# Kernel tuning notes

Measured on AMD Instinct MI355X. Metric: run time of the kernel, lower is better.

The kernel has to match this reference:

```python
import jax, jax.numpy as jnp
import numpy as np

C = 512
NUM_HEADS = 8
NUM_GROUPS = 32
EPS = 1e-6


def group_norm(x, gamma, beta):
    # x: [B, C, N]
    b, c, n = x.shape
    xg = x.reshape(b, NUM_GROUPS, (c // NUM_GROUPS) * n)
    mean = xg.mean(axis=-1, keepdims=True)
    var = xg.var(axis=-1, keepdims=True)
    xg = (xg - mean) * jax.lax.rsqrt(var + EPS)
    x = xg.reshape(b, c, n)
    return x * gamma[None, :, None] + beta[None, :, None]


def conv1x1(x, w, bias):
    # pointwise conv: w [out_c, in_c], x [B, C, N]
    return jnp.einsum('oc,bcn->bon', w, x) + bias[None, :, None]


def setup_inputs() -> dict:
    key = jax.random.key(0)
    ks = jax.random.split(key, 11)
    s = 1.0 / np.sqrt(C)
    inp = {
        'x': jax.random.normal(ks[0], (4, C, 2048), dtype=jnp.float32),
        'gn_gamma': jnp.ones((C,), jnp.float32),
        'gn_beta': jnp.zeros((C,), jnp.float32),
        'q_w': jax.random.uniform(ks[1], (C, C), jnp.float32, -s, s),
        'q_b': jax.random.uniform(ks[2], (C,), jnp.float32, -s, s),
        'k_w': jax.random.uniform(ks[3], (C, C), jnp.float32, -s, s),
        'k_b': jax.random.uniform(ks[4], (C,), jnp.float32, -s, s),
        'v_w': jax.random.uniform(ks[5], (C, C), jnp.float32, -s, s),
        'v_b': jax.random.uniform(ks[6], (C,), jnp.float32, -s, s),
        'proj_w': jax.random.uniform(ks[7], (C, C), jnp.float32, -s, s),
        'proj_b': jax.random.uniform(ks[8], (C,), jnp.float32, -s, s),
    }
    return inp


def reference(x, gn_gamma, gn_beta, q_w, q_b, k_w, k_b, v_w, v_b, proj_w, proj_b):
    b, c, n = x.shape
    hc = c // NUM_HEADS
    h_ = group_norm(x, gn_gamma, gn_beta)
    q = conv1x1(h_, q_w, q_b)
    k = conv1x1(h_, k_w, k_b)
    v = conv1x1(h_, v_w, v_b)
    # split heads: [B, H, hc, N]
    q = q.reshape(b, NUM_HEADS, hc, n)
    k = k.reshape(b, NUM_HEADS, hc, n)
    v = v.reshape(b, NUM_HEADS, hc, n)
    # NOTE: scale uses full channel count c, matching the original code
    scale = jnp.asarray(c, x.dtype) ** -0.5
    # scores: [B, H, Nq, Nk]
    w = jnp.einsum('bhcn,bhcm->bhnm', q, k) * scale
    w = jax.nn.softmax(w, axis=-1)
    # out[b,h,c,q] = sum_m v[b,h,c,m] * w[b,h,q,m]
    out = jnp.einsum('bhcm,bhqm->bhcq', v, w)
    out = out.reshape(b, c, n)
    out = conv1x1(out, proj_w, proj_b)
    return x + out
```

## Files before the change

### kernel.cpp

```cpp
#include <hip/hip_runtime.h>
#include <hip/hip_bf16.h>
#include <math.h>

#define C_DIM 512
#define N_DIM 2048
#define B_DIM 4
#define NGRP 32
#define GCH 16
#define NHEAD 8
#define HDIM 64
#define EPSV 1e-6f

using f32x4  = __attribute__((ext_vector_type(4))) float;
using bf16x8 = __attribute__((ext_vector_type(8))) short;

#define GLL16(gp, lp) __builtin_amdgcn_global_load_lds( \
    (const __attribute__((address_space(1))) unsigned int*)(gp), \
    (__attribute__((address_space(3))) unsigned int*)(lp), 16, 0, 0)

#define BFPACK(a, b) __builtin_amdgcn_perm(__float_as_uint(b), __float_as_uint(a), 0x07060302u)

static __device__ __forceinline__ unsigned short f2bf(float f) {
    union { __hip_bfloat16 h; unsigned short u; } cv;
    cv.h = __float2bfloat16(f);
    return cv.u;
}

__global__ __launch_bounds__(256) void gn_stats(const float* __restrict__ x,
                                                float* __restrict__ partial) {
    const int HSZ = GCH * N_DIM / 2;
    int blk = blockIdx.x;
    const float4* x4 = (const float4*)(x + (size_t)blk * HSZ);
    int tid = threadIdx.x;

    float s = 0.f, ss = 0.f;
    #pragma unroll
    for (int it = 0; it < HSZ / 4 / 256; ++it) {
        float4 v = x4[tid + it * 256];
        s  += v.x + v.y + v.z + v.w;
        ss += v.x * v.x + v.y * v.y + v.z * v.z + v.w * v.w;
    }
    __shared__ float rs[256], rss[256];
    rs[tid] = s; rss[tid] = ss;
    __syncthreads();
    for (int off = 128; off > 0; off >>= 1) {
        if (tid < off) { rs[tid] += rs[tid + off]; rss[tid] += rss[tid + off]; }
        __syncthreads();
    }
    if (tid == 0) {
        partial[blk * 2]     = rs[0];
        partial[blk * 2 + 1] = rss[0];
    }
}

__global__ __launch_bounds__(256) void gn_apply_t(const float* __restrict__ x,
                                                  const float* __restrict__ partial,
                                                  const float* __restrict__ gamma,
                                                  const float* __restrict__ beta,
                                                  unsigned short* __restrict__ ht) {
    __shared__ char smem[8192];
    const float GSZI = 1.f / (GCH * N_DIM);
    int n0 = blockIdx.x * 64, c0 = blockIdx.y * 64, b = blockIdx.z;
    int tid = threadIdx.x;
    #pragma unroll
    for (int it = 0; it < 4; ++it) {
        int idx = tid + it * 256;
        int ci = idx >> 4, n4 = (idx & 15) << 2;
        int cg = c0 + ci, grp = cg >> 4;
        int bg = b * NGRP + grp;
        float s  = partial[bg * 4]     + partial[bg * 4 + 2];
        float ss = partial[bg * 4 + 1] + partial[bg * 4 + 3];
        float mean = s * GSZI;
        float var  = ss * GSZI - mean * mean;
        float rstd = rsqrtf(var + EPSV);
        float ga = gamma[cg] * rstd, be = beta[cg] - mean * ga;
        float4 v = *(const float4*)&x[((size_t)b * C_DIM + cg) * N_DIM + n0 + n4];
        float vals[4] = {v.x, v.y, v.z, v.w};
        #pragma unroll
        for (int j = 0; j < 4; ++j) {
            int nl = n4 + j;
            *(unsigned short*)(smem + nl * 128 + ((ci * 2) ^ ((nl & 7) << 4))) =
                f2bf(vals[j] * ga + be);
        }
    }
    __syncthreads();
    #pragma unroll
    for (int i = 0; i < 2; ++i) {
        int idx = tid + i * 256;
        int row = idx >> 3, ch = idx & 7;
        bf16x8 v = *(const bf16x8*)(smem + row * 128 + ((ch * 16) ^ ((row & 7) << 4)));
        *(bf16x8*)&ht[((size_t)(b * N_DIM + n0 + row)) * C_DIM + c0 + ch * 8] = v;
    }
}

__global__ __launch_bounds__(256) void cast4_bf16(const float* __restrict__ s0,
                                                  const float* __restrict__ s1,
                                                  const float* __restrict__ s2,
                                                  const float* __restrict__ s3,
                                                  unsigned short* __restrict__ dst) {
    int which = blockIdx.y;
    const float* src = (which == 0) ? s0 : (which == 1) ? s1 : (which == 2) ? s2 : s3;
    size_t idx = (size_t)blockIdx.x * 256 + threadIdx.x;
    const float4* s4 = (const float4*)src;
    float4 a = s4[idx * 2], b = s4[idx * 2 + 1];
    bf16x8 o;
    o[0] = (short)f2bf(a.x); o[1] = (short)f2bf(a.y);
    o[2] = (short)f2bf(a.z); o[3] = (short)f2bf(a.w);
    o[4] = (short)f2bf(b.x); o[5] = (short)f2bf(b.y);
    o[6] = (short)f2bf(b.z); o[7] = (short)f2bf(b.w);
    *(bf16x8*)&dst[(size_t)which * 262144 + idx * 8] = o;
}

__global__ __launch_bounds__(512) void conv_qkv(const unsigned short* __restrict__ Wall,
                                                const float* __restrict__ q_b,
                                                const float* __restrict__ k_b,
                                                const float* __restrict__ v_b,
                                                const unsigned short* __restrict__ ht,
                                                unsigned short* __restrict__ qt,
                                                unsigned short* __restrict__ kt,
                                                unsigned short* __restrict__ vt,
                                                float escale) {
    __shared__ char smem[40960];

    int bn0 = blockIdx.x * 128;
    int bo  = blockIdx.y * 64;
    int tid = threadIdx.x;
    int L = tid & 63, w = tid >> 6;
    int g = L >> 4, c = L & 15;
    int wr = w >> 2, wc = w & 3;

    f32x4 acc[3][2][2];
    #pragma unroll
    for (int w3 = 0; w3 < 3; ++w3)
        #pragma unroll
        for (int t = 0; t < 2; ++t)
            #pragma unroll
            for (int u = 0; u < 2; ++u) acc[w3][t][u] = f32x4{0.f, 0.f, 0.f, 0.f};

    for (int k0 = 0; k0 < C_DIM; k0 += 64) {
        if (w < 4) {
            #pragma unroll
            for (int i = 0; i < 4; ++i) {
                int j = w * 4 + i;
                int row = j * 8 + (L >> 3);
                int sl = (L & 7) ^ (row & 7);
                GLL16(ht + (size_t)(bn0 + row) * C_DIM + k0 + sl * 8, smem + j * 1024);
            }
        } else {
            #pragma unroll
            for (int i = 0; i < 6; ++i) {
                int j = (w - 4) * 6 + i;
                int w3 = j >> 3, jj = j & 7;
                int row = jj * 8 + (L >> 3);
                int sl = (L & 7) ^ (row & 7);
                GLL16(Wall + (size_t)w3 * 262144 + (size_t)(bo + row) * C_DIM + k0 + sl * 8,
                      smem + 16384 + j * 1024);
            }
        }
        __syncthreads();

        bf16x8 bfr[2][2];
        #pragma unroll
        for (int u = 0; u < 2; ++u) {
            int row = wc * 32 + u * 16 + c;
            #pragma unroll
            for (int ks = 0; ks < 2; ++ks)
                bfr[u][ks] = *(const bf16x8*)(smem + row * 128 +
                                              ((g * 16 + ks * 64) ^ ((row & 7) << 4)));
        }
        #pragma unroll
        for (int w3 = 0; w3 < 3; ++w3) {
            char* As = smem + 16384 + w3 * 8192;
            bf16x8 af[2][2];
            #pragma unroll
            for (int t = 0; t < 2; ++t) {
                int row = wr * 32 + t * 16 + c;
                #pragma unroll
                for (int ks = 0; ks < 2; ++ks)
                    af[t][ks] = *(const bf16x8*)(As + row * 128 +
                                                 ((g * 16 + ks * 64) ^ ((row & 7) << 4)));
            }
            #pragma unroll
            for (int ks = 0; ks < 2; ++ks)
                #pragma unroll
                for (int t = 0; t < 2; ++t)
                    #pragma unroll
                    for (int u = 0; u < 2; ++u)
                        acc[w3][t][u] = __builtin_amdgcn_mfma_f32_16x16x32_bf16(
                            af[t][ks], bfr[u][ks], acc[w3][t][u], 0, 0, 0);
        }
        __syncthreads();
    }

    int b  = bn0 >> 11;
    int nb = bn0 & (N_DIM - 1);
    int hh = bo >> 6;
    int bh = b * NHEAD + hh;

    #pragma unroll
    for (int t = 0; t < 2; ++t)
        #pragma unroll
        for (int r = 0; r < 4; ++r) {
            int m = bo + wr * 32 + t * 16 + g * 4 + r;
            float bi = v_b[m];
            #pragma unroll
            for (int u = 0; u < 2; ++u) {
                int n = nb + wc * 32 + u * 16 + c;
                vt[((size_t)b * C_DIM + m) * N_DIM + n] = f2bf(acc[2][t][u][r] + bi);
            }
        }

    char* Ts = smem;
    #pragma unroll
    for (int pass = 0; pass < 2; ++pass) {
        const float* bias = pass ? k_b : q_b;
        float esc = pass ? 1.0f : escale;
        unsigned short* dst = pass ? kt : qt;
        __syncthreads();
        #pragma unroll
        for (int t = 0; t < 2; ++t)
            #pragma unroll
            for (int r = 0; r < 4; ++r) {
                int ml = wr * 32 + t * 16 + g * 4 + r;
                float bi = bias[bo + ml];
                #pragma unroll
                for (int u = 0; u < 2; ++u) {
                    int nl = wc * 32 + u * 16 + c;
                    *(unsigned short*)(Ts + nl * 128 + ((ml * 2) ^ ((nl & 7) << 4))) =
                        f2bf((acc[pass][t][u][r] + bi) * esc);
                }
            }
        __syncthreads();
        #pragma unroll
        for (int i = 0; i < 2; ++i) {
            int idx = tid + i * 512;
            int row = idx >> 3, ch = idx & 7;
            bf16x8 v = *(const bf16x8*)(Ts + row * 128 + ((ch * 16) ^ ((row & 7) << 4)));
            *(bf16x8*)&dst[((size_t)bh * N_DIM + nb + row) * HDIM + ch * 8] = v;
        }
    }
}

__global__ __launch_bounds__(256) void conv_proj(const unsigned short* __restrict__ Wb,
                                                 const float* __restrict__ bias,
                                                 const unsigned short* __restrict__ Bsrc,
                                                 const float* __restrict__ res,
                                                 float* __restrict__ outf) {
    __shared__ char smem[24576];
    int bn0 = blockIdx.x * 128;
    int bo  = blockIdx.y * 64;
    int tid = threadIdx.x;
    int L = tid & 63, w = tid >> 6;
    int g = L >> 4, c = L & 15;
    int wr = w >> 1, wc = w & 1;

    f32x4 acc[2][4];
    #pragma unroll
    for (int t = 0; t < 2; ++t)
        #pragma unroll
        for (int u = 0; u < 4; ++u) acc[t][u] = f32x4{0.f, 0.f, 0.f, 0.f};

    for (int k0 = 0; k0 < C_DIM; k0 += 64) {
        #pragma unroll
        for (int i = 0; i < 2; ++i) {
            int j = w * 2 + i;
            int ra = j * 8 + (L >> 3);
            int sl = (L & 7) ^ (ra & 7);
            GLL16(Wb + (size_t)(bo + ra) * C_DIM + k0 + sl * 8, smem + j * 1024);
        }
        #pragma unroll
        for (int i = 0; i < 4; ++i) {
            int j = w * 4 + i;
            int rb = j * 8 + (L >> 3);
            int sl = (L & 7) ^ (rb & 7);
            GLL16(Bsrc + (size_t)(bn0 + rb) * C_DIM + k0 + sl * 8, smem + 8192 + j * 1024);
        }
        __syncthreads();

        bf16x8 af[2][2], bfr[4][2];
        #pragma unroll
        for (int t = 0; t < 2; ++t) {
            int row = wr * 32 + t * 16 + c;
            #pragma unroll
            for (int ks = 0; ks < 2; ++ks)
                af[t][ks] = *(const bf16x8*)(smem + row * 128 +
                                             ((g * 16 + ks * 64) ^ ((row & 7) << 4)));
        }
        #pragma unroll
        for (int u = 0; u < 4; ++u) {
            int row = wc * 64 + u * 16 + c;
            #pragma unroll
            for (int ks = 0; ks < 2; ++ks)
                bfr[u][ks] = *(const bf16x8*)(smem + 8192 + row * 128 +
                                              ((g * 16 + ks * 64) ^ ((row & 7) << 4)));
        }
        #pragma unroll
        for (int ks = 0; ks < 2; ++ks)
            #pragma unroll
            for (int t = 0; t < 2; ++t)
                #pragma unroll
                for (int u = 0; u < 4; ++u)
                    acc[t][u] = __builtin_amdgcn_mfma_f32_16x16x32_bf16(
                        af[t][ks], bfr[u][ks], acc[t][u], 0, 0, 0);
        __syncthreads();
    }

    int b  = bn0 >> 11;
    int nb = bn0 & (N_DIM - 1);
    #pragma unroll
    for (int t = 0; t < 2; ++t)
        #pragma unroll
        for (int r = 0; r < 4; ++r) {
            int m = bo + wr * 32 + t * 16 + g * 4 + r;
            float bi = bias[m];
            #pragma unroll
            for (int u = 0; u < 4; ++u) {
                int n = nb + wc * 64 + u * 16 + c;
                size_t off = ((size_t)b * C_DIM + m) * N_DIM + n;
                outf[off] = acc[t][u][r] + bi + res[off];
            }
        }
}

__global__ __launch_bounds__(512, 4) void attn_kernel(const unsigned short* __restrict__ Qt,
                                                      const unsigned short* __restrict__ Kt,
                                                      const unsigned short* __restrict__ Vt,
                                                      unsigned short* __restrict__ at) {
    __shared__ char smem[49152];

    int d = blockIdx.x;
    int xcd = d & 7;
    int slot = d >> 3;
    int bh = xcd + 8 * (slot >> 4);
    int q0 = (slot & 15) * 128;

    int b = bh >> 3, hh = bh & 7;
    int tid = threadIdx.x;
    int L = tid & 63, w = tid >> 6;
    int g = L >> 4, c = L & 15;

    const unsigned short* Qh = Qt + (size_t)bh * N_DIM * HDIM;
    const unsigned short* Kh = Kt + (size_t)bh * N_DIM * HDIM;
    const unsigned short* Vh = Vt + (size_t)bh * HDIM * N_DIM;

    #pragma unroll
    for (int i = 0; i < 2; ++i) {
        int j = w * 2 + i;
        int row = j * 8 + (L >> 3);
        int sl = (L & 7) ^ (row & 7);
        GLL16(Qh + (size_t)(q0 + row) * HDIM + sl * 8, smem + j * 1024);
    }
    int srow = w * 8 + (L >> 3);
    int ssl  = (L & 7) ^ (srow & 7);
    GLL16(Kh + (size_t)srow * HDIM + ssl * 8, smem + 16384 + w * 1024);
    GLL16(Vh + (size_t)srow * N_DIM + ssl * 8, smem + 24576 + w * 1024);
    __syncthreads();

    int csw = (c & 7) << 4;
    char* kb0 = smem + 16384 + c * 128 + ((g * 16) ^ csw);
    char* kb1 = smem + 16384 + c * 128 + ((g * 16 + 64) ^ csw);
    char* pb  = smem + (w * 16 + c) * 128;
    char* pw0 = pb + ((g * 8) ^ csw);
    char* pw1 = pb + ((32 + g * 8) ^ csw);
    char* pw2 = pb + ((64 + g * 8) ^ csw);
    char* pw3 = pb + ((96 + g * 8) ^ csw);
    char* pr0 = pb + ((g * 16) ^ csw);
    char* pr1 = pb + ((64 + g * 16) ^ csw);

    bf16x8 qf[2];
    qf[0] = *(const bf16x8*)pr0;
    qf[1] = *(const bf16x8*)pr1;

    const unsigned short* kgp = Kh + (size_t)(64 + srow) * HDIM + ssl * 8;
    const unsigned short* vgp = Vh + (size_t)srow * N_DIM + 64 + ssl * 8;

    f32x4 oacc[4];
    #pragma unroll
    for (int t = 0; t < 4; ++t) oacc[t] = f32x4{0.f, 0.f, 0.f, 0.f};
    float m_r = -INFINITY, l_part = 0.f;

    auto tile = [&](int BOFF) {
        f32x4 sacc[4];
        #pragma unroll
        for (int t = 0; t < 4; ++t) sacc[t] = f32x4{0.f, 0.f, 0.f, 0.f};
        __builtin_amdgcn_s_setprio(1);
        #pragma unroll
        for (int t = 0; t < 4; ++t) {
            bf16x8 kf0 = *(const bf16x8*)(kb0 + BOFF + t * 2048);
            bf16x8 kf1 = *(const bf16x8*)(kb1 + BOFF + t * 2048);
            sacc[t] = __builtin_amdgcn_mfma_f32_16x16x32_bf16(kf0, qf[0], sacc[t], 0, 0, 0);
            sacc[t] = __builtin_amdgcn_mfma_f32_16x16x32_bf16(kf1, qf[1], sacc[t], 0, 0, 0);
        }
        __builtin_amdgcn_s_setprio(0);

        float t0 = fmaxf(fmaxf(sacc[0][0], sacc[0][1]), sacc[0][2]);
        float t1 = fmaxf(fmaxf(sacc[0][3], sacc[1][0]), sacc[1][1]);
        float t2 = fmaxf(fmaxf(sacc[1][2], sacc[1][3]), sacc[2][0]);
        float t3 = fmaxf(fmaxf(sacc[2][1], sacc[2][2]), sacc[2][3]);
        float t4 = fmaxf(fmaxf(sacc[3][0], sacc[3][1]), sacc[3][2]);
        float mloc = fmaxf(fmaxf(fmaxf(t0, t1), fmaxf(t2, t3)), fmaxf(t4, sacc[3][3]));
        if (!__all(mloc - m_r <= 6.0f)) {
            mloc = fmaxf(mloc, __shfl_xor(mloc, 16));
            mloc = fmaxf(mloc, __shfl_xor(mloc, 32));
            float mn = fmaxf(m_r, mloc);
            float fac = exp2f(m_r - mn);
            m_r = mn;
            l_part *= fac;
            #pragma unroll
            for (int t = 0; t < 4; ++t) oacc[t] = oacc[t] * fac;
        }
        f32x4 m4 = {m_r, m_r, m_r, m_r};
        f32x4 p[4];
        #pragma unroll
        for (int t = 0; t < 4; ++t) {
            f32x4 dd = sacc[t] - m4;
            p[t][0] = exp2f(dd[0]);
            p[t][1] = exp2f(dd[1]);
            p[t][2] = exp2f(dd[2]);
            p[t][3] = exp2f(dd[3]);
        }
        f32x4 racc = (p[0] + p[1]) + (p[2] + p[3]);
        l_part += (racc[0] + racc[1]) + (racc[2] + racc[3]);

        unsigned pk[4][2];
        #pragma unroll
        for (int t = 0; t < 4; ++t) {
            pk[t][0] = BFPACK(p[t][0], p[t][1]);
            pk[t][1] = BFPACK(p[t][2], p[t][3]);
        }

        *(unsigned long long*)pw0 = (unsigned long long)pk[0][0] | ((unsigned long long)pk[0][1] << 32);
        *(unsigned long long*)pw1 = (unsigned long long)pk[1][0] | ((unsigned long long)pk[1][1] << 32);
        *(unsigned long long*)pw2 = (unsigned long long)pk[2][0] | ((unsigned long long)pk[2][1] << 32);
        *(unsigned long long*)pw3 = (unsigned long long)pk[3][0] | ((unsigned long long)pk[3][1] << 32);

        __builtin_amdgcn_s_setprio(1);
        {
            bf16x8 pf0 = *(const bf16x8*)pr0;
            #pragma unroll
            for (int t = 0; t < 4; ++t) {
                bf16x8 vf = *(const bf16x8*)(kb0 + BOFF + 8192 + t * 2048);
                oacc[t] = __builtin_amdgcn_mfma_f32_16x16x32_bf16(vf, pf0, oacc[t], 0, 0, 0);
            }
            bf16x8 pf1 = *(const bf16x8*)pr1;
            #pragma unroll
            for (int t = 0; t < 4; ++t) {
                bf16x8 vf = *(const bf16x8*)(kb1 + BOFF + 8192 + t * 2048);
                oacc[t] = __builtin_amdgcn_mfma_f32_16x16x32_bf16(vf, pf1, oacc[t], 0, 0, 0);
            }
        }
        __builtin_amdgcn_s_setprio(0);
    };

    for (int i = 0; i < 16; ++i) {
        GLL16(kgp, smem + 32768 + w * 1024);
        GLL16(vgp, smem + 40960 + w * 1024);
        kgp += 64 * HDIM;
        vgp += 64;
        tile(0);
        __syncthreads();
        if (i < 15) {
            GLL16(kgp, smem + 16384 + w * 1024);
            GLL16(vgp, smem + 24576 + w * 1024);
            kgp += 64 * HDIM;
            vgp += 64;
        }
        tile(16384);
        __syncthreads();
    }

    float l_r = l_part;
    l_r += __shfl_xor(l_r, 16);
    l_r += __shfl_xor(l_r, 32);
    float oinv = 1.f / l_r;
    {
        unsigned lo, hi;
        lo = BFPACK(oacc[0][0] * oinv, oacc[0][1] * oinv);
        hi = BFPACK(oacc[0][2] * oinv, oacc[0][3] * oinv);
        *(unsigned long long*)pw0 = (unsigned long long)lo | ((unsigned long long)hi << 32);
        lo = BFPACK(oacc[1][0] * oinv, oacc[1][1] * oinv);
        hi = BFPACK(oacc[1][2] * oinv, oacc[1][3] * oinv);
        *(unsigned long long*)pw1 = (unsigned long long)lo | ((unsigned long long)hi << 32);
        lo = BFPACK(oacc[2][0] * oinv, oacc[2][1] * oinv);
        hi = BFPACK(oacc[2][2] * oinv, oacc[2][3] * oinv);
        *(unsigned long long*)pw2 = (unsigned long long)lo | ((unsigned long long)hi << 32);
        lo = BFPACK(oacc[3][0] * oinv, oacc[3][1] * oinv);
        hi = BFPACK(oacc[3][2] * oinv, oacc[3][3] * oinv);
        *(unsigned long long*)pw3 = (unsigned long long)lo | ((unsigned long long)hi << 32);
    }
    char* wbase = smem + w * 2048;
    #pragma unroll
    for (int i = 0; i < 2; ++i) {
        int idx = L + i * 64;
        int row = idx >> 3, ch = idx & 7;
        bf16x8 v = *(const bf16x8*)(wbase + row * 128 + ((ch * 16) ^ ((row & 7) << 4)));
        *(bf16x8*)&at[((size_t)(b * N_DIM + q0 + w * 16 + row)) * C_DIM + hh * HDIM + ch * 8] = v;
    }
}

extern "C" void kernel_launch(void* const* d_in, const int* in_sizes, int n_in,
                              void* d_out, int out_size, void* d_ws, size_t ws_size,
                              hipStream_t stream) {
    (void)in_sizes; (void)n_in; (void)out_size; (void)ws_size;
    const float* x     = (const float*)d_in[0];
    const float* gam   = (const float*)d_in[1];
    const float* bet   = (const float*)d_in[2];
    const float* q_w   = (const float*)d_in[3];
    const float* q_b   = (const float*)d_in[4];
    const float* k_w   = (const float*)d_in[5];
    const float* k_b   = (const float*)d_in[6];
    const float* v_w   = (const float*)d_in[7];
    const float* v_b   = (const float*)d_in[8];
    const float* p_w   = (const float*)d_in[9];
    const float* p_b   = (const float*)d_in[10];
    float* out = (float*)d_out;

    const size_t MB = 1 << 20;
    char* wsb = (char*)d_ws;
    unsigned short* ht  = (unsigned short*)(wsb);
    unsigned short* wqb = (unsigned short*)(wsb + 8 * MB);
    unsigned short* wpb = (unsigned short*)(wsb + 9 * MB + 512 * 1024);
    float*          partial = (float*)(wsb + 10 * MB);
    unsigned short* qt  = (unsigned short*)(wsb + 11 * MB);
    unsigned short* kt  = (unsigned short*)(wsb + 19 * MB);
    unsigned short* vt  = (unsigned short*)(wsb + 27 * MB);
    unsigned short* at  = (unsigned short*)(wsb + 35 * MB);

    gn_stats<<<B_DIM * NGRP * 2, 256, 0, stream>>>(x, partial);
    gn_apply_t<<<dim3(N_DIM / 64, C_DIM / 64, B_DIM), 256, 0, stream>>>(x, partial, gam, bet, ht);

    cast4_bf16<<<dim3(128, 4), 256, 0, stream>>>(q_w, k_w, v_w, p_w, wqb);

    const float escale = 0.044194173824159216f * 1.4426950408889634f;
    conv_qkv<<<dim3(B_DIM * N_DIM / 128, C_DIM / 64), 512, 0, stream>>>(
        wqb, q_b, k_b, v_b, ht, qt, kt, vt, escale);

    attn_kernel<<<512, 512, 0, stream>>>(qt, kt, vt, at);

    conv_proj<<<dim3(B_DIM * N_DIM / 128, C_DIM / 64), 256, 0, stream>>>(wpb, p_b, at, x, out);
}
```

Before: 113.5 us.

## Software-pipeline attention: overlap next QK^T MFMA with softmax/PV via triple buffering

Restructures the attention loop so that the QK^T MFMAs for the next key tile are issued alongside the PV MFMAs of the current tile, with the softmax done between them. K/V shared-memory staging moves from double to triple buffering (LDS grows from 48KB to 64KB), using explicit vmcnt waits and raw barriers in place of __syncthreads. The exp2f and reciprocal calls are replaced with the raw hardware intrinsics. The larger LDS footprint may lower occupancy from 4 blocks per CU, and the manual waitcnt and barrier logic adds correctness risk.

Result: faster. 101.7 us (-10.5%).

```diff
diff --git a/kernel.cpp b/kernel.cpp
--- a/kernel.cpp
+++ b/kernel.cpp
@@ -19,6 +19,8 @@
     (__attribute__((address_space(3))) unsigned int*)(lp), 16, 0, 0)
 
 #define BFPACK(a, b) __builtin_amdgcn_perm(__float_as_uint(b), __float_as_uint(a), 0x07060302u)
+
+#define EXP2R(x) __builtin_amdgcn_exp2f(x)
 
 static __device__ __forceinline__ unsigned short f2bf(float f) {
     union { __hip_bfloat16 h; unsigned short u; } cv;
@@ -326,7 +328,7 @@
                                                       const unsigned short* __restrict__ Kt,
                                                       const unsigned short* __restrict__ Vt,
                                                       unsigned short* __restrict__ at) {
-    __shared__ char smem[49152];
+    __shared__ char smem[65536];
 
     int d = blockIdx.x;
     int xcd = d & 7;
@@ -352,13 +354,15 @@
     }
     int srow = w * 8 + (L >> 3);
     int ssl  = (L & 7) ^ (srow & 7);
-    GLL16(Kh + (size_t)srow * HDIM + ssl * 8, smem + 16384 + w * 1024);
-    GLL16(Vh + (size_t)srow * N_DIM + ssl * 8, smem + 24576 + w * 1024);
+    GLL16(Kh + (size_t)srow * HDIM + ssl * 8,         smem + 16384 + w * 1024);
+    GLL16(Vh + (size_t)srow * N_DIM + ssl * 8,        smem + 24576 + w * 1024);
+    GLL16(Kh + (size_t)(64 + srow) * HDIM + ssl * 8,  smem + 32768 + w * 1024);
+    GLL16(Vh + (size_t)srow * N_DIM + 64 + ssl * 8,   smem + 40960 + w * 1024);
     __syncthreads();
 
     int csw = (c & 7) << 4;
-    char* kb0 = smem + 16384 + c * 128 + ((g * 16) ^ csw);
-    char* kb1 = smem + 16384 + c * 128 + ((g * 16 + 64) ^ csw);
+    char* kb0 = smem + c * 128 + ((g * 16) ^ csw);
+    char* kb1 = smem + c * 128 + ((g * 16 + 64) ^ csw);
     char* pb  = smem + (w * 16 + c) * 128;
     char* pw0 = pb + ((g * 8) ^ csw);
     char* pw1 = pb + ((32 + g * 8) ^ csw);
@@ -371,28 +375,15 @@
     qf[0] = *(const bf16x8*)pr0;
     qf[1] = *(const bf16x8*)pr1;
 
-    const unsigned short* kgp = Kh + (size_t)(64 + srow) * HDIM + ssl * 8;
-    const unsigned short* vgp = Vh + (size_t)srow * N_DIM + 64 + ssl * 8;
+    const unsigned short* kgp = Kh + (size_t)(128 + srow) * HDIM + ssl * 8;
+    const unsigned short* vgp = Vh + (size_t)srow * N_DIM + 128 + ssl * 8;
 
     f32x4 oacc[4];
     #pragma unroll
     for (int t = 0; t < 4; ++t) oacc[t] = f32x4{0.f, 0.f, 0.f, 0.f};
     float m_r = -INFINITY, l_part = 0.f;
 
-    auto tile = [&](int BOFF) {
-        f32x4 sacc[4];
-        #pragma unroll
-        for (int t = 0; t < 4; ++t) sacc[t] = f32x4{0.f, 0.f, 0.f, 0.f};
-        __builtin_amdgcn_s_setprio(1);
-        #pragma unroll
-        for (int t = 0; t < 4; ++t) {
-            bf16x8 kf0 = *(const bf16x8*)(kb0 + BOFF + t * 2048);
-            bf16x8 kf1 = *(const bf16x8*)(kb1 + BOFF + t * 2048);
-            sacc[t] = __builtin_amdgcn_mfma_f32_16x16x32_bf16(kf0, qf[0], sacc[t], 0, 0, 0);
-            sacc[t] = __builtin_amdgcn_mfma_f32_16x16x32_bf16(kf1, qf[1], sacc[t], 0, 0, 0);
-        }
-        __builtin_amdgcn_s_setprio(0);
-
+    auto smx = [&](f32x4 (&sacc)[4]) {
         float t0 = fmaxf(fmaxf(sacc[0][0], sacc[0][1]), sacc[0][2]);
         float t1 = fmaxf(fmaxf(sacc[0][3], sacc[1][0]), sacc[1][1]);
         float t2 = fmaxf(fmaxf(sacc[1][2], sacc[1][3]), sacc[2][0]);
@@ -403,7 +394,7 @@
             mloc = fmaxf(mloc, __shfl_xor(mloc, 16));
             mloc = fmaxf(mloc, __shfl_xor(mloc, 32));
             float mn = fmaxf(m_r, mloc);
-            float fac = exp2f(m_r - mn);
+            float fac = EXP2R(m_r - mn);
             m_r = mn;
             l_part *= fac;
             #pragma unroll
@@ -414,10 +405,10 @@
         #pragma unroll
         for (int t = 0; t < 4; ++t) {
             f32x4 dd = sacc[t] - m4;
-            p[t][0] = exp2f(dd[0]);
-            p[t][1] = exp2f(dd[1]);
-            p[t][2] = exp2f(dd[2]);
-            p[t][3] = exp2f(dd[3]);
+            p[t][0] = EXP2R(dd[0]);
+            p[t][1] = EXP2R(dd[1]);
+            p[t][2] = EXP2R(dd[2]);
+            p[t][3] = EXP2R(dd[3]);
         }
         f32x4 racc = (p[0] + p[1]) + (p[2] + p[3]);
         l_part += (racc[0] + racc[1]) + (racc[2] + racc[3]);
@@ -428,51 +419,85 @@
             pk[t][0] = BFPACK(p[t][0], p[t][1]);
             pk[t][1] = BFPACK(p[t][2], p[t][3]);
         }
-
         *(unsigned long long*)pw0 = (unsigned long long)pk[0][0] | ((unsigned long long)pk[0][1] << 32);
         *(unsigned long long*)pw1 = (unsigned long long)pk[1][0] | ((unsigned long long)pk[1][1] << 32);
         *(unsigned long long*)pw2 = (unsigned long long)pk[2][0] | ((unsigned long long)pk[2][1] << 32);
         *(unsigned long long*)pw3 = (unsigned long long)pk[3][0] | ((unsigned long long)pk[3][1] << 32);
+    };
+
+    f32x4 sA[4], sB[4];
+    #pragma unroll
+    for (int t = 0; t < 4; ++t) sA[t] = f32x4{0.f, 0.f, 0.f, 0.f};
+    #pragma unroll
+    for (int t = 0; t < 4; ++t) {
+        bf16x8 kf0 = *(const bf16x8*)(kb0 + 16384 + t * 2048);
+        bf16x8 kf1 = *(const bf16x8*)(kb1 + 16384 + t * 2048);
+        sA[t] = __builtin_amdgcn_mfma_f32_16x16x32_bf16(kf0, qf[0], sA[t], 0, 0, 0);
+        sA[t] = __builtin_amdgcn_mfma_f32_16x16x32_bf16(kf1, qf[1], sA[t], 0, 0, 0);
+    }
+
+    auto step = [&](f32x4 (&sCur)[4], f32x4 (&sNxt)[4], int vboff, int kboff, int stoff) {
+        smx(sCur);
+        __builtin_amdgcn_s_barrier();
+        asm volatile("" ::: "memory");
+        if (stoff >= 0) {
+            GLL16(kgp, smem + stoff + w * 1024);
+            GLL16(vgp, smem + stoff + 8192 + w * 1024);
+            kgp += 64 * HDIM;
+            vgp += 64;
+            asm volatile("s_waitcnt vmcnt(2)" ::: "memory");
+        } else {
+            asm volatile("s_waitcnt vmcnt(0)" ::: "memory");
+        }
+        __builtin_amdgcn_sched_barrier(0);
 
         __builtin_amdgcn_s_setprio(1);
-        {
-            bf16x8 pf0 = *(const bf16x8*)pr0;
-            #pragma unroll
-            for (int t = 0; t < 4; ++t) {
-                bf16x8 vf = *(const bf16x8*)(kb0 + BOFF + 8192 + t * 2048);
-                oacc[t] = __builtin_amdgcn_mfma_f32_16x16x32_bf16(vf, pf0, oacc[t], 0, 0, 0);
-            }
-            bf16x8 pf1 = *(const bf16x8*)pr1;
-            #pragma unroll
-            for (int t = 0; t < 4; ++t) {
-                bf16x8 vf = *(const bf16x8*)(kb1 + BOFF + 8192 + t * 2048);
-                oacc[t] = __builtin_amdgcn_mfma_f32_16x16x32_bf16(vf, pf1, oacc[t], 0, 0, 0);
-            }
+        #pragma unroll
+        for (int t = 0; t < 4; ++t) sNxt[t] = f32x4{0.f, 0.f, 0.f, 0.f};
+        bf16x8 pf0 = *(const bf16x8*)pr0;
+        bf16x8 pf1 = *(const bf16x8*)pr1;
+        #pragma unroll
+        for (int t = 0; t < 4; ++t) {
+            bf16x8 kf0 = *(const bf16x8*)(kb0 + kboff + t * 2048);
+            bf16x8 kf1 = *(const bf16x8*)(kb1 + kboff + t * 2048);
+            sNxt[t] = __builtin_amdgcn_mfma_f32_16x16x32_bf16(kf0, qf[0], sNxt[t], 0, 0, 0);
+            sNxt[t] = __builtin_amdgcn_mfma_f32_16x16x32_bf16(kf1, qf[1], sNxt[t], 0, 0, 0);
+            bf16x8 vf0 = *(const bf16x8*)(kb0 + vboff + 8192 + t * 2048);
+            bf16x8 vf1 = *(const bf16x8*)(kb1 + vboff + 8192 + t * 2048);
+            oacc[t] = __builtin_amdgcn_mfma_f32_16x16x32_bf16(vf0, pf0, oacc[t], 0, 0, 0);
+            oacc[t] = __builtin_amdgcn_mfma_f32_16x16x32_bf16(vf1, pf1, oacc[t], 0, 0, 0);
         }
         __builtin_amdgcn_s_setprio(0);
     };
 
-    for (int i = 0; i < 16; ++i) {
-        GLL16(kgp, smem + 32768 + w * 1024);
-        GLL16(vgp, smem + 40960 + w * 1024);
-        kgp += 64 * HDIM;
-        vgp += 64;
-        tile(0);
-        __syncthreads();
-        if (i < 15) {
-            GLL16(kgp, smem + 16384 + w * 1024);
-            GLL16(vgp, smem + 24576 + w * 1024);
-            kgp += 64 * HDIM;
-            vgp += 64;
-        }
-        tile(16384);
-        __syncthreads();
+    int vb = 16384, kb = 32768, st = 49152;
+    for (int ii = 0; ii < 15; ++ii) {
+        step(sA, sB, vb, kb, st);
+        { int t_ = vb; vb = kb; kb = st; st = t_; }
+        step(sB, sA, vb, kb, st);
+        { int t_ = vb; vb = kb; kb = st; st = t_; }
+    }
+    step(sA, sB, vb, kb, -1);
+    { int t_ = vb; vb = kb; kb = st; st = t_; }
+    {
+        smx(sB);
+        bf16x8 pf0 = *(const bf16x8*)pr0;
+        bf16x8 pf1 = *(const bf16x8*)pr1;
+        __builtin_amdgcn_s_setprio(1);
+        #pragma unroll
+        for (int t = 0; t < 4; ++t) {
+            bf16x8 vf0 = *(const bf16x8*)(kb0 + vb + 8192 + t * 2048);
+            bf16x8 vf1 = *(const bf16x8*)(kb1 + vb + 8192 + t * 2048);
+            oacc[t] = __builtin_amdgcn_mfma_f32_16x16x32_bf16(vf0, pf0, oacc[t], 0, 0, 0);
+            oacc[t] = __builtin_amdgcn_mfma_f32_16x16x32_bf16(vf1, pf1, oacc[t], 0, 0, 0);
+        }
+        __builtin_amdgcn_s_setprio(0);
     }
 
     float l_r = l_part;
     l_r += __shfl_xor(l_r, 16);
     l_r += __shfl_xor(l_r, 32);
-    float oinv = 1.f / l_r;
+    float oinv = __builtin_amdgcn_rcpf(l_r);
     {
         unsigned lo, hi;
         lo = BFPACK(oacc[0][0] * oinv, oacc[0][1] * oinv);
```
